# Optimization experiments

Measured on AMD Instinct MI355X. Metric: run time of the kernel, lower is better.

Reference implementation:

```python
import jax, jax.numpy as jnp
import numpy as np

E = 524288
IN = 256
OUT = 256
T = 16


def setup_inputs() -> dict:
    key = jax.random.key(0)
    k1, k2, k3 = jax.random.split(key, 3)
    x_j = jax.random.normal(k1, (E, IN), dtype=jnp.float32)
    # kaiming-uniform-ish init for the per-type weights
    bound = 1.0 / np.sqrt(IN)
    rel_weights = jax.random.uniform(k2, (T, IN, OUT), dtype=jnp.float32,
                                     minval=-bound, maxval=bound)
    edge_types = jax.random.randint(k3, (E,), 0, T, dtype=jnp.int64)
    return {"x_j": x_j, "rel_weights": rel_weights, "edge_types": edge_types}


def reference(x_j, rel_weights, edge_types):
    # Faithful to the torch semantics:
    #   out[i] = x_j[edge_types[i]] @ rel_weights[edge_types[i]]
    # (the torch code's broadcasted matmul + [i, edge_types[i]] gather reduces
    #  to a per-type matvec followed by an index gather).
    num_types = rel_weights.shape[0]
    # y[t] = x_j[t] @ W[t], shape [T, OUT] -- tiny compute
    y = jnp.einsum('ti,tio->to', x_j[:num_types], rel_weights)
    # memory-bound gather to [E, OUT]
    return y[edge_types]
```

## Files before the change

### kernel.cpp

```cpp
#include <hip/hip_runtime.h>


#define RL_IN  256
#define RL_OUT 256
#define RL_T   16

typedef float f32x4 __attribute__((ext_vector_type(4)));

__global__ __launch_bounds__(1024)
void rl_compute_y(const float* __restrict__ x,
                  const float* __restrict__ W,
                  float* __restrict__ y) {
    const int t = blockIdx.x;
    const int c = threadIdx.x >> 8;
    const int o = threadIdx.x & 255;
    const int i0 = c * 64;

    __shared__ float xs[RL_IN];
    if (threadIdx.x < RL_IN) xs[threadIdx.x] = x[t * RL_IN + threadIdx.x];
    __syncthreads();

    const float* Wt = W + (size_t)t * RL_IN * RL_OUT + (size_t)i0 * RL_OUT;
    float acc = 0.0f;
#pragma unroll 8
    for (int i = 0; i < 64; ++i) {
        acc += xs[i0 + i] * Wt[i * RL_OUT + o];
    }

    __shared__ float part[4][RL_OUT];
    part[c][o] = acc;
    __syncthreads();
    if (c == 0) {
        y[t * RL_OUT + o] = part[0][o] + part[1][o] + part[2][o] + part[3][o];
    }
}

__global__ __launch_bounds__(256)
void rl_gather(const int* __restrict__ et,
               const f32x4* __restrict__ y4,
               f32x4* __restrict__ out4,
               int E) {
    __shared__ f32x4 ys[RL_T * (RL_OUT / 4)];
    __shared__ int tys[256];

    for (int i = threadIdx.x; i < RL_T * (RL_OUT / 4); i += blockDim.x)
        ys[i] = y4[i];
    __syncthreads();

    const int lane       = threadIdx.x & 63;
    const int waveBase   = threadIdx.x & ~63;
    const int wave       = blockIdx.x * (blockDim.x >> 6) + (threadIdx.x >> 6);
    const int totalWaves = gridDim.x * (blockDim.x >> 6);

    for (int base = wave * 64; base < E; base += totalWaves * 64) {
        tys[waveBase + lane] = et[base + lane];

        if (base + 64 <= E) {
#pragma unroll 8
            for (int r = 0; r < 64; ++r) {
                const int t = tys[waveBase + r];
                f32x4 v = ys[t * 64 + lane];
                __builtin_nontemporal_store(
                    v, &out4[(size_t)(base + r) * 64 + lane]);
            }
        } else {
            for (int r = 0; base + r < E; ++r) {
                const int t = tys[waveBase + r];
                f32x4 v = ys[t * 64 + lane];
                __builtin_nontemporal_store(
                    v, &out4[(size_t)(base + r) * 64 + lane]);
            }
        }
    }
}

extern "C" void kernel_launch(void* const* d_in, const int* in_sizes, int n_in,
                              void* d_out, int out_size, void* d_ws, size_t ws_size,
                              hipStream_t stream) {
    const float* x_j  = (const float*)d_in[0];
    const float* W    = (const float*)d_in[1];
    const int*   et   = (const int*)d_in[2];
    float*       out  = (float*)d_out;

    const int E = in_sizes[2];

    float* y = (float*)d_ws;

    rl_compute_y<<<RL_T, 1024, 0, stream>>>(x_j, W, y);

    rl_gather<<<2048, 256, 0, stream>>>(et, (const f32x4*)y,
                                        (f32x4*)out, E);
}
```

Before: 103.4 us.

## Widen gather spans to 512 rows with int4 index loads and fewer blocks

Each wave now handles 512 consecutive output rows instead of 64. The type indices for a span are loaded as int4 vectors into per-wave shared memory. Output stores become ordinary stores rather than nontemporal ones, and the grid drops from 2048 to 256 blocks. The aim is to cut per-iteration index-load overhead and give each wave longer contiguous write streams, at the risk of lower occupancy and different cache behaviour on the large output write.

```diff
diff --git a/kernel.cpp b/kernel.cpp
--- a/kernel.cpp
+++ b/kernel.cpp
@@ -35,40 +35,43 @@
     }
 }
 
+#define SPAN 512
+
 __global__ __launch_bounds__(256)
 void rl_gather(const int* __restrict__ et,
                const f32x4* __restrict__ y4,
                f32x4* __restrict__ out4,
                int E) {
     __shared__ f32x4 ys[RL_T * (RL_OUT / 4)];
-    __shared__ int tys[256];
+    __shared__ int tys[4][SPAN];
 
     for (int i = threadIdx.x; i < RL_T * (RL_OUT / 4); i += blockDim.x)
         ys[i] = y4[i];
+
+    const int lane = threadIdx.x & 63;
+    const int w    = threadIdx.x >> 6;
+    const int gw   = blockIdx.x * 4 + w;
+    const int nW   = gridDim.x * 4;
+
     __syncthreads();
 
-    const int lane       = threadIdx.x & 63;
-    const int waveBase   = threadIdx.x & ~63;
-    const int wave       = blockIdx.x * (blockDim.x >> 6) + (threadIdx.x >> 6);
-    const int totalWaves = gridDim.x * (blockDim.x >> 6);
+    const int4* et4 = (const int4*)et;
 
-    for (int base = wave * 64; base < E; base += totalWaves * 64) {
-        tys[waveBase + lane] = et[base + lane];
-
-        if (base + 64 <= E) {
+    for (long base = (long)gw * SPAN; base < E; base += (long)nW * SPAN) {
+        if (base + SPAN <= E) {
+            int4* t4 = (int4*)tys[w];
+            t4[lane]      = et4[base / 4 + lane];
+            t4[64 + lane] = et4[base / 4 + 64 + lane];
+            size_t o0 = (size_t)base * 64 + lane;
 #pragma unroll 8
-            for (int r = 0; r < 64; ++r) {
-                const int t = tys[waveBase + r];
-                f32x4 v = ys[t * 64 + lane];
-                __builtin_nontemporal_store(
-                    v, &out4[(size_t)(base + r) * 64 + lane]);
+            for (int r = 0; r < SPAN; ++r) {
+                const int t = tys[w][r];
+                out4[o0 + (size_t)r * 64] = ys[t * 64 + lane];
             }
         } else {
-            for (int r = 0; base + r < E; ++r) {
-                const int t = tys[waveBase + r];
-                f32x4 v = ys[t * 64 + lane];
-                __builtin_nontemporal_store(
-                    v, &out4[(size_t)(base + r) * 64 + lane]);
+            for (long row = base; row < E; ++row) {
+                const int t = et[row];
+                out4[(size_t)row * 64 + lane] = ys[t * 64 + lane];
             }
         }
     }
@@ -88,6 +91,6 @@
 
     rl_compute_y<<<RL_T, 1024, 0, stream>>>(x_j, W, y);
 
-    rl_gather<<<2048, 256, 0, stream>>>(et, (const f32x4*)y,
-                                        (f32x4*)out, E);
+    rl_gather<<<256, 256, 0, stream>>>(et, (const f32x4*)y,
+                                       (f32x4*)out, E);
 }
```

Result: slower. 113.9 us (+10.2%).
